# Kernel optimization log

Hardware: AMD Instinct MI355X
Metric: run time of the kernel (lower is better)

The kernel has to match this reference:

```python
import jax, jax.numpy as jnp
import numpy as np

N_NODES = 100000
LN_EPS = 1e-5
NEG_SLOPE = 0.2


def setup_inputs() -> dict:
    key = jax.random.key(0)
    ks = jax.random.split(key, 6)
    N, E, NIN, EDIM, NOUT, H = N_NODES, 1600000, 64, 32, 128, 4
    x = jax.random.normal(ks[0], (N, NIN), dtype=jnp.float32)
    edge_index = jax.random.randint(ks[1], (2, E), 0, N, dtype=jnp.int64)
    edge_attr = jax.random.normal(ks[2], (E, EDIM), dtype=jnp.float32)
    # xavier-uniform linear weights (torch layout: [out, in])
    def xavier(k, fan_out, fan_in):
        lim = float(np.sqrt(6.0 / (fan_in + fan_out)))
        return jax.random.uniform(k, (fan_out, fan_in), jnp.float32, -lim, lim)
    W_msg = xavier(ks[3], NOUT, NIN + EDIM)          # (128, 96)
    W_att = xavier(ks[4], H, 2 * NIN + EDIM)         # (4, 160)
    bias = jnp.zeros((NOUT,), jnp.float32)
    ln_gamma = jnp.ones((NOUT,), jnp.float32)
    ln_beta = jnp.zeros((NOUT,), jnp.float32)
    return {"x": x, "edge_index": edge_index, "edge_attr": edge_attr,
            "W_msg": W_msg, "W_att": W_att, "bias": bias,
            "ln_gamma": ln_gamma, "ln_beta": ln_beta}


def reference(x, edge_index, edge_attr, W_msg, W_att, bias, ln_gamma, ln_beta):
    N = x.shape[0]
    H = W_att.shape[0]
    src, dst = edge_index[0], edge_index[1]
    xs = x[src]                                       # (E, node_in) gather
    xd = x[dst]                                       # (E, node_in) gather
    # message: W_msg @ [h_u ; x_uv]
    msg_in = jnp.concatenate([xs, edge_attr], axis=-1)            # (E, 96)
    msgs = msg_in @ W_msg.T                                        # (E, out_dim)
    msgs = msgs.reshape(-1, H, W_msg.shape[0] // H)                # (E, H, D)
    # attention logits: LeakyReLU(W_att @ [h_u ; h_v ; x_uv])
    att_in = jnp.concatenate([xs, xd, edge_attr], axis=-1)         # (E, 160)
    logits = att_in @ W_att.T                                      # (E, H)
    logits = jax.nn.leaky_relu(logits, NEG_SLOPE)
    # per-destination-node sparse softmax
    seg_max = jax.ops.segment_max(logits, dst, num_segments=N)     # (N, H)
    exp_l = jnp.exp(logits - seg_max[dst])                         # (E, H)
    seg_sum = jax.ops.segment_sum(exp_l, dst, num_segments=N)      # (N, H)
    att = exp_l / (seg_sum[dst] + 1e-9)                            # (E, H)
    # weighted scatter-add aggregation
    weighted = msgs * att[..., None]                               # (E, H, D)
    out = jax.ops.segment_sum(weighted, dst, num_segments=N)       # (N, H, D)
    out = out.reshape(N, -1) + bias                                # concat heads
    # layer norm over feature dim
    mu = out.mean(axis=-1, keepdims=True)
    var = out.var(axis=-1, keepdims=True)
    out = (out - mu) * jax.lax.rsqrt(var + LN_EPS) * ln_gamma + ln_beta
    return out
```

## Files before the change

kernel.cpp:

```cpp
#include <hip/hip_runtime.h>
#include <hip/hip_bf16.h>

typedef __attribute__((ext_vector_type(8))) short short8;
typedef __attribute__((ext_vector_type(4))) float f32x4;

__device__ __forceinline__ unsigned short fbf(float f) {
  union { float f; unsigned u; } v; v.f = f;
  unsigned r = v.u + 0x7fffu + ((v.u >> 16) & 1u);
  return (unsigned short)(r >> 16);
}
__device__ __forceinline__ unsigned pk2(float a, float b) {
  return (unsigned)fbf(a) | ((unsigned)fbf(b) << 16);
}
__device__ __forceinline__ float ubf(unsigned hi) {
  union { unsigned u; float f; } v; v.u = hi << 16; return v.f;
}
__device__ __forceinline__ float dot4(float4 a, float4 b) {
  return fmaf(a.x, b.x, fmaf(a.y, b.y, fmaf(a.z, b.z, a.w * b.w)));
}

__launch_bounds__(256)
__global__ void k_phase1(const float* __restrict__ x, const float* __restrict__ W_att,
                         const int* __restrict__ edst, int E,
                         float4* __restrict__ A_s, float4* __restrict__ A_d,
                         unsigned* __restrict__ xb32, int* __restrict__ deg, int N) {
  __shared__ float4 s_wa[160];
  if (threadIdx.x < 160) s_wa[threadIdx.x] = ((const float4*)W_att)[threadIdx.x];
  for (int i = blockIdx.x * blockDim.x + threadIdx.x; i < E; i += gridDim.x * blockDim.x)
    atomicAdd(&deg[edst[i]], 1);
  __syncthreads();
  for (int v = blockIdx.x * blockDim.x + threadIdx.x; v < N; v += gridDim.x * blockDim.x) {
    const float4* xp = (const float4*)&x[v * 64];
    float4 xq[16];
    #pragma unroll
    for (int k = 0; k < 16; k++) xq[k] = xp[k];
    float as[4] = {}, ad[4] = {};
    #pragma unroll
    for (int h = 0; h < 4; h++) {
      #pragma unroll
      for (int k = 0; k < 16; k++) {
        as[h] += dot4(s_wa[h * 40 + k], xq[k]);
        ad[h] += dot4(s_wa[h * 40 + 16 + k], xq[k]);
      }
    }
    A_s[v] = make_float4(as[0], as[1], as[2], as[3]);
    A_d[v] = make_float4(ad[0], ad[1], ad[2], ad[3]);
    #pragma unroll
    for (int k = 0; k < 16; k++) {
      xb32[v * 32 + 2 * k]     = pk2(xq[k].x, xq[k].y);
      xb32[v * 32 + 2 * k + 1] = pk2(xq[k].z, xq[k].w);
    }
  }
}

__global__ void k_scan1(const int* __restrict__ deg, int N, int* __restrict__ part,
                        int* __restrict__ bsum) {
  __shared__ int tmp[1024];
  int tid = threadIdx.x;
  int i = blockIdx.x * 1024 + tid;
  int dv = (i < N) ? deg[i] : 0;
  int v = (dv + 7) & ~7;
  tmp[tid] = v;
  __syncthreads();
  for (int ofs = 1; ofs < 1024; ofs <<= 1) {
    int t = (tid >= ofs) ? tmp[tid - ofs] : 0;
    __syncthreads();
    tmp[tid] += t;
    __syncthreads();
  }
  if (i < N) part[i] = tmp[tid] - v;
  if (tid == 1023) bsum[blockIdx.x] = tmp[tid];
}

__global__ void k_scan2(int* __restrict__ part, const int* __restrict__ bsum,
                        const int* __restrict__ deg, int N, int* __restrict__ cursor) {
  __shared__ int sbase;
  if (threadIdx.x == 0) {
    int b = 0;
    for (int j = 0; j < (int)blockIdx.x; j++) b += bsum[j];
    sbase = b;
  }
  __syncthreads();
  int i = blockIdx.x * 1024 + threadIdx.x;
  if (i < N) {
    int o = part[i] + sbase;
    part[i] = o;
    cursor[i] = o;
    if (i == N - 1) part[N] = o + ((deg[i] + 7) & ~7);
  }
}

__launch_bounds__(256)
__global__ void k_fill2(const int* __restrict__ esrc, const int* __restrict__ edst, int E,
                        const float* __restrict__ ea, const float4* __restrict__ A_s,
                        const float4* __restrict__ A_d, const float* __restrict__ W_att,
                        int* __restrict__ cursor, int2* __restrict__ csr2,
                        float4* __restrict__ attc) {
  __shared__ float4 s_we[32];
  if (threadIdx.x < 32) {
    int h = threadIdx.x >> 3, k4 = threadIdx.x & 7;
    const float* p = &W_att[h * 160 + 128 + k4 * 4];
    s_we[threadIdx.x] = make_float4(p[0], p[1], p[2], p[3]);
  }
  __syncthreads();
  for (int e = blockIdx.x * blockDim.x + threadIdx.x; e < E; e += gridDim.x * blockDim.x) {
    const int s = esrc[e], d = edst[e];
    const int slot = atomicAdd(&cursor[d], 1);
    const float4* ep = (const float4*)&ea[(unsigned)e * 32u];
    float4 eq[8];
    #pragma unroll
    for (int k = 0; k < 8; k++) eq[k] = ep[k];
    const float4 as4 = A_s[s], ad4 = A_d[d];
    const float base[4] = {as4.x + ad4.x, as4.y + ad4.y, as4.z + ad4.z, as4.w + ad4.w};
    float av[4];
    #pragma unroll
    for (int h = 0; h < 4; h++) {
      float lg = base[h];
      #pragma unroll
      for (int k = 0; k < 8; k++) lg += dot4(s_we[h * 8 + k], eq[k]);
      lg = fmaxf(lg, 0.2f * lg);
      av[h] = __expf(lg);
    }
    attc[slot] = make_float4(av[0], av[1], av[2], av[3]);
    csr2[slot] = make_int2(s, e);
  }
}

__launch_bounds__(256)
__global__ void k_agg2(const unsigned short* __restrict__ xb, const float* __restrict__ ea,
                       const int2* __restrict__ csr2, const float4* __restrict__ attc,
                       const int* __restrict__ offsets,
                       unsigned short* __restrict__ agg, float* __restrict__ denom, int N) {
  __shared__ int2 s_ids[4][32];
  const int lane = threadIdx.x & 63;
  const int wvb = threadIdx.x >> 6;
  const int wv = (blockIdx.x * blockDim.x + threadIdx.x) >> 6;
  const int nw = (gridDim.x * blockDim.x) >> 6;
  const int l32 = lane & 31;
  const bool hi = lane >= 32;

  for (int v0 = wv; v0 < N; v0 += nw) {
    const int vv = __builtin_amdgcn_readfirstlane(v0);
    const int sstart = __builtin_amdgcn_readfirstlane(offsets[vv]);
    const int send = __builtin_amdgcn_readfirstlane(offsets[vv + 1]);
    const int ng = (send - sstart) >> 3;

    float ax0 = 0, ax1 = 0, ax2 = 0, ax3 = 0;
    float ae0 = 0, ae1 = 0, ae2 = 0, ae3 = 0;
    float dn0 = 0, dn1 = 0, dn2 = 0, dn3 = 0;

    if (ng > 0) {
      {
        int2 q_ = csr2[sstart + l32];
        if (lane < 32) s_ids[wvb][l32] = q_;
      }
      for (int g = 0; g < ng; g++) {
        if (g > 0 && (g & 3) == 0) {
          int2 q_ = csr2[sstart + g * 8 + l32];
          if (lane < 32) s_ids[wvb][l32] = q_;
        }
        const int qo = (g & 3) * 8;
        const float4* ap8 = &attc[sstart + g * 8];
        const float4 at0 = ap8[0], at1 = ap8[1], at2 = ap8[2], at3 = ap8[3];
        const float4 at4 = ap8[4], at5 = ap8[5], at6 = ap8[6], at7 = ap8[7];
        const int2 t0 = s_ids[wvb][qo + 0], t1 = s_ids[wvb][qo + 1];
        const int2 t2 = s_ids[wvb][qo + 2], t3 = s_ids[wvb][qo + 3];
        const int2 t4 = s_ids[wvb][qo + 4], t5 = s_ids[wvb][qo + 5];
        const int2 t6 = s_ids[wvb][qo + 6], t7 = s_ids[wvb][qo + 7];
        const unsigned short q0 = xb[(unsigned)(t0.x << 6) + lane];
        const unsigned short q1 = xb[(unsigned)(t1.x << 6) + lane];
        const unsigned short q2 = xb[(unsigned)(t2.x << 6) + lane];
        const unsigned short q3 = xb[(unsigned)(t3.x << 6) + lane];
        const unsigned short q4 = xb[(unsigned)(t4.x << 6) + lane];
        const unsigned short q5 = xb[(unsigned)(t5.x << 6) + lane];
        const unsigned short q6 = xb[(unsigned)(t6.x << 6) + lane];
        const unsigned short q7 = xb[(unsigned)(t7.x << 6) + lane];
        const float e0 = ea[(unsigned)(t0.y << 5) + l32];
        const float e1 = ea[(unsigned)(t1.y << 5) + l32];
        const float e2 = ea[(unsigned)(t2.y << 5) + l32];
        const float e3 = ea[(unsigned)(t3.y << 5) + l32];
        const float e4 = ea[(unsigned)(t4.y << 5) + l32];
        const float e5 = ea[(unsigned)(t5.y << 5) + l32];
        const float e6 = ea[(unsigned)(t6.y << 5) + l32];
        const float e7 = ea[(unsigned)(t7.y << 5) + l32];
        float xf;
#define ACC(AT, Q, EV)                                                      \
        xf = ubf((unsigned)Q);                                              \
        ax0 = fmaf(AT.x, xf, ax0); ax1 = fmaf(AT.y, xf, ax1);               \
        ax2 = fmaf(AT.z, xf, ax2); ax3 = fmaf(AT.w, xf, ax3);               \
        ae0 = fmaf(AT.x, EV, ae0); ae1 = fmaf(AT.y, EV, ae1);               \
        ae2 = fmaf(AT.z, EV, ae2); ae3 = fmaf(AT.w, EV, ae3);               \
        dn0 += AT.x; dn1 += AT.y; dn2 += AT.z; dn3 += AT.w;
        ACC(at0, q0, e0) ACC(at1, q1, e1) ACC(at2, q2, e2) ACC(at3, q3, e3)
        ACC(at4, q4, e4) ACC(at5, q5, e5) ACC(at6, q6, e6) ACC(at7, q7, e7)
#undef ACC
      }
    }

    const unsigned base = (unsigned)v0 * 384u;
    agg[base + lane]        = fbf(ax0);
    agg[base + 96 + lane]   = fbf(ax1);
    agg[base + 192 + lane]  = fbf(ax2);
    agg[base + 288 + lane]  = fbf(ax3);
    const int hA = hi ? 2 : 0;
    agg[base + hA * 96 + 64 + l32]       = fbf(hi ? ae2 : ae0);
    agg[base + (hA + 1) * 96 + 64 + l32] = fbf(hi ? ae3 : ae1);
    if (lane == 0) ((float4*)denom)[v0] = make_float4(dn0, dn1, dn2, dn3);
  }
}

__launch_bounds__(128)
__global__ void k_out(const unsigned short* __restrict__ agg, const float* __restrict__ W_msg,
                      const float* __restrict__ denom, const float* __restrict__ bias,
                      const float* __restrict__ gamma, const float* __restrict__ beta,
                      float* __restrict__ out, int N, int T) {
  __shared__ float s_den[64];
  __shared__ float s_sum[2][16], s_sq[2][16];
  const int f = threadIdx.x;
  const int w = f >> 6;
  const int l = f & 63;
  const int c16 = l & 15;
  const int rg = l >> 4;

  short8 wb[2][2][3];
  float biasv[2][2], gv[2][2], bv[2][2];
  #pragma unroll
  for (int hh = 0; hh < 2; hh++) {
    const int head = 2 * w + hh;
    #pragma unroll
    for (int ct = 0; ct < 2; ct++) {
      const int q = head * 32 + ct * 16 + c16;
      biasv[hh][ct] = bias[q]; gv[hh][ct] = gamma[q]; bv[hh][ct] = beta[q];
      #pragma unroll
      for (int kk = 0; kk < 3; kk++) {
        const float* p = &W_msg[q * 96 + kk * 32 + rg * 8];
        short8 s;
        #pragma unroll
        for (int i = 0; i < 8; i++) s[i] = (short)fbf(p[i]);
        wb[hh][ct][kk] = s;
      }
    }
  }

  for (int t = blockIdx.x; t < T; t += gridDim.x) {
    const int n0 = t * 16;
    if (f < 64) s_den[f] = denom[min(n0 + (f >> 2), N - 1) * 4 + (f & 3)];
    __syncthreads();

    f32x4 c[2][2] = {{{0.f,0.f,0.f,0.f},{0.f,0.f,0.f,0.f}},
                     {{0.f,0.f,0.f,0.f},{0.f,0.f,0.f,0.f}}};
    const int nA = min(n0 + c16, N - 1);
    #pragma unroll
    for (int hh = 0; hh < 2; hh++) {
      const int head = 2 * w + hh;
      #pragma unroll
      for (int kk = 0; kk < 3; kk++) {
        short8 a = *(const short8*)&agg[nA * 384 + head * 96 + kk * 32 + rg * 8];
        c[hh][0] = __builtin_amdgcn_mfma_f32_16x16x32_bf16(a, wb[hh][0][kk], c[hh][0], 0, 0, 0);
        c[hh][1] = __builtin_amdgcn_mfma_f32_16x16x32_bf16(a, wb[hh][1][kk], c[hh][1], 0, 0, 0);
      }
    }

    float val[2][2][4];
    #pragma unroll
    for (int hh = 0; hh < 2; hh++)
      #pragma unroll
      for (int ct = 0; ct < 2; ct++)
        #pragma unroll
        for (int r = 0; r < 4; r++) {
          const float d = s_den[(rg * 4 + r) * 4 + (2 * w + hh)] + 1e-9f;
          val[hh][ct][r] = c[hh][ct][r] / d + biasv[hh][ct];
        }

    float sr[4], qr[4];
    #pragma unroll
    for (int r = 0; r < 4; r++) {
      float s = 0.f, q2 = 0.f;
      #pragma unroll
      for (int hh = 0; hh < 2; hh++)
        #pragma unroll
        for (int ct = 0; ct < 2; ct++) { s += val[hh][ct][r]; q2 = fmaf(val[hh][ct][r], val[hh][ct][r], q2); }
      #pragma unroll
      for (int m = 1; m <= 8; m <<= 1) { s += __shfl_xor(s, m, 64); q2 += __shfl_xor(q2, m, 64); }
      sr[r] = s; qr[r] = q2;
    }
    if (c16 == 0) {
      #pragma unroll
      for (int r = 0; r < 4; r++) { s_sum[w][rg * 4 + r] = sr[r]; s_sq[w][rg * 4 + r] = qr[r]; }
    }
    __syncthreads();

    float mean[4], rstd[4];
    #pragma unroll
    for (int r = 0; r < 4; r++) {
      const int ni = rg * 4 + r;
      mean[r] = (s_sum[0][ni] + s_sum[1][ni]) * (1.f / 128.f);
      const float m2 = (s_sq[0][ni] + s_sq[1][ni]) * (1.f / 128.f);
      rstd[r] = rsqrtf(m2 - mean[r] * mean[r] + 1e-5f);
    }
    #pragma unroll
    for (int hh = 0; hh < 2; hh++)
      #pragma unroll
      for (int ct = 0; ct < 2; ct++)
        #pragma unroll
        for (int r = 0; r < 4; r++) {
          const int n = n0 + rg * 4 + r;
          if (n < N)
            out[n * 128 + (2 * w + hh) * 32 + ct * 16 + c16] =
                (val[hh][ct][r] - mean[r]) * rstd[r] * gv[hh][ct] + bv[hh][ct];
        }
    __syncthreads();
  }
}

extern "C" void kernel_launch(void* const* d_in, const int* in_sizes, int n_in,
                              void* d_out, int out_size, void* d_ws, size_t ws_size,
                              hipStream_t stream) {
  const float* x     = (const float*)d_in[0];
  const int*   ei    = (const int*)d_in[1];
  const float* ea    = (const float*)d_in[2];
  const float* W_msg = (const float*)d_in[3];
  const float* W_att = (const float*)d_in[4];
  const float* bias  = (const float*)d_in[5];
  const float* gamma = (const float*)d_in[6];
  const float* beta  = (const float*)d_in[7];
  float* out = (float*)d_out;

  const int N = in_sizes[0] / 64;
  const int E = in_sizes[1] / 2;
  const int* esrc = ei;
  const int* edst = ei + E;
  const int EP = E + 8 * N + 64;

  char* p = (char*)d_ws;
  int* deg      = (int*)p;            p += (size_t)N * 4;
  int* offsets  = (int*)p;            p += (size_t)(N + 1) * 4;
  int* cursor   = (int*)p;            p += (size_t)N * 4;
  int* bsum     = (int*)p;            p += 2048 * 4;
  int2* csr2    = (int2*)p;           p += (size_t)EP * 8;
  float4* attc  = (float4*)p;         p += (size_t)EP * 16;
  float4* A_s   = (float4*)p;         p += (size_t)N * 16;
  float4* A_d   = (float4*)p;         p += (size_t)N * 16;
  unsigned short* xb = (unsigned short*)p; p += (size_t)N * 64 * 2;
  unsigned short* agg = (unsigned short*)p; p += (size_t)N * 384 * 2;
  float* denom  = (float*)p;

  hipMemsetAsync(deg, 0, (size_t)N * 4, stream);
  hipMemsetAsync(csr2, 0, (size_t)EP * 8, stream);
  hipMemsetAsync(attc, 0, (size_t)EP * 16, stream);
  const int SB = (N + 1023) / 1024;
  const int T = (N + 15) / 16;

  k_phase1<<<2048, 256, 0, stream>>>(x, W_att, edst, E, A_s, A_d, (unsigned*)xb, deg, N);
  k_scan1<<<SB, 1024, 0, stream>>>(deg, N, offsets, bsum);
  k_scan2<<<SB, 1024, 0, stream>>>(offsets, bsum, deg, N, cursor);
  k_fill2<<<2048, 256, 0, stream>>>(esrc, edst, E, ea, A_s, A_d, W_att, cursor, csr2, attc);
  k_agg2<<<2048, 256, 0, stream>>>(xb, ea, csr2, attc, offsets, agg, denom, N);
  k_out<<<T, 128, 0, stream>>>(agg, W_msg, denom, bias, gamma, beta, out, N, T);
}
```

Before: 437.0 us.

## Store attention weights in edge order and pad CSR slots with a sentinel

The fill kernel now writes exp-attention per original edge id (coalesced) instead of scattering into CSR slot order. The aggregation kernel gathers it through the stored edge id. A small pad kernel fills the padding slots with a sentinel edge whose attention is zero, which replaces two large memsets of the CSR and attention buffers. This trades coalesced reads in aggregation for gathered 16-byte reads, while removing scattered writes and memset traffic.

Result: slower. 462.0 us (+5.7%).

```diff
diff --git a/kernel.cpp b/kernel.cpp
--- a/kernel.cpp
+++ b/kernel.cpp
@@ -90,12 +90,24 @@
   }
 }
 
+__global__ void k_pad(const int* __restrict__ offsets, const int* __restrict__ deg,
+                      int2* __restrict__ csr2, float4* __restrict__ att_eo,
+                      int N, int E) {
+  int v = blockIdx.x * blockDim.x + threadIdx.x;
+  if (v == 0) att_eo[E] = make_float4(0.f, 0.f, 0.f, 0.f);
+  if (v < N) {
+    const int o = offsets[v], d = deg[v];
+    const int pe = o + ((d + 7) & ~7);
+    for (int s = o + d; s < pe; s++) csr2[s] = make_int2(0, E);
+  }
+}
+
 __launch_bounds__(256)
-__global__ void k_fill2(const int* __restrict__ esrc, const int* __restrict__ edst, int E,
+__global__ void k_fill3(const int* __restrict__ esrc, const int* __restrict__ edst, int E,
                         const float* __restrict__ ea, const float4* __restrict__ A_s,
                         const float4* __restrict__ A_d, const float* __restrict__ W_att,
                         int* __restrict__ cursor, int2* __restrict__ csr2,
-                        float4* __restrict__ attc) {
+                        float4* __restrict__ att_eo) {
   __shared__ float4 s_we[32];
   if (threadIdx.x < 32) {
     int h = threadIdx.x >> 3, k4 = threadIdx.x & 7;
@@ -121,14 +133,14 @@
       lg = fmaxf(lg, 0.2f * lg);
       av[h] = __expf(lg);
     }
-    attc[slot] = make_float4(av[0], av[1], av[2], av[3]);
+    att_eo[e] = make_float4(av[0], av[1], av[2], av[3]);
     csr2[slot] = make_int2(s, e);
   }
 }
 
 __launch_bounds__(256)
 __global__ void k_agg2(const unsigned short* __restrict__ xb, const float* __restrict__ ea,
-                       const int2* __restrict__ csr2, const float4* __restrict__ attc,
+                       const int2* __restrict__ csr2, const float4* __restrict__ att_eo,
                        const int* __restrict__ offsets,
                        unsigned short* __restrict__ agg, float* __restrict__ denom, int N) {
   __shared__ int2 s_ids[4][32];
@@ -160,13 +172,18 @@
           if (lane < 32) s_ids[wvb][l32] = q_;
         }
         const int qo = (g & 3) * 8;
-        const float4* ap8 = &attc[sstart + g * 8];
-        const float4 at0 = ap8[0], at1 = ap8[1], at2 = ap8[2], at3 = ap8[3];
-        const float4 at4 = ap8[4], at5 = ap8[5], at6 = ap8[6], at7 = ap8[7];
         const int2 t0 = s_ids[wvb][qo + 0], t1 = s_ids[wvb][qo + 1];
         const int2 t2 = s_ids[wvb][qo + 2], t3 = s_ids[wvb][qo + 3];
         const int2 t4 = s_ids[wvb][qo + 4], t5 = s_ids[wvb][qo + 5];
         const int2 t6 = s_ids[wvb][qo + 6], t7 = s_ids[wvb][qo + 7];
+        const float4 at0 = att_eo[(unsigned)t0.y];
+        const float4 at1 = att_eo[(unsigned)t1.y];
+        const float4 at2 = att_eo[(unsigned)t2.y];
+        const float4 at3 = att_eo[(unsigned)t3.y];
+        const float4 at4 = att_eo[(unsigned)t4.y];
+        const float4 at5 = att_eo[(unsigned)t5.y];
+        const float4 at6 = att_eo[(unsigned)t6.y];
+        const float4 at7 = att_eo[(unsigned)t7.y];
         const unsigned short q0 = xb[(unsigned)(t0.x << 6) + lane];
         const unsigned short q1 = xb[(unsigned)(t1.x << 6) + lane];
         const unsigned short q2 = xb[(unsigned)(t2.x << 6) + lane];
@@ -338,7 +355,7 @@
   int* cursor   = (int*)p;            p += (size_t)N * 4;
   int* bsum     = (int*)p;            p += 2048 * 4;
   int2* csr2    = (int2*)p;           p += (size_t)EP * 8;
-  float4* attc  = (float4*)p;         p += (size_t)EP * 16;
+  float4* att_eo = (float4*)p;        p += (size_t)(E + 8) * 16;
   float4* A_s   = (float4*)p;         p += (size_t)N * 16;
   float4* A_d   = (float4*)p;         p += (size_t)N * 16;
   unsigned short* xb = (unsigned short*)p; p += (size_t)N * 64 * 2;
@@ -346,15 +363,14 @@
   float* denom  = (float*)p;
 
   hipMemsetAsync(deg, 0, (size_t)N * 4, stream);
-  hipMemsetAsync(csr2, 0, (size_t)EP * 8, stream);
-  hipMemsetAsync(attc, 0, (size_t)EP * 16, stream);
   const int SB = (N + 1023) / 1024;
   const int T = (N + 15) / 16;
 
   k_phase1<<<2048, 256, 0, stream>>>(x, W_att, edst, E, A_s, A_d, (unsigned*)xb, deg, N);
   k_scan1<<<SB, 1024, 0, stream>>>(deg, N, offsets, bsum);
   k_scan2<<<SB, 1024, 0, stream>>>(offsets, bsum, deg, N, cursor);
-  k_fill2<<<2048, 256, 0, stream>>>(esrc, edst, E, ea, A_s, A_d, W_att, cursor, csr2, attc);
-  k_agg2<<<2048, 256, 0, stream>>>(xb, ea, csr2, attc, offsets, agg, denom, N);
+  k_pad<<<(N + 255) / 256, 256, 0, stream>>>(offsets, deg, csr2, att_eo, N, E);
+  k_fill3<<<2048, 256, 0, stream>>>(esrc, edst, E, ea, A_s, A_d, W_att, cursor, csr2, att_eo);
+  k_agg2<<<2048, 256, 0, stream>>>(xb, ea, csr2, att_eo, offsets, agg, denom, N);
   k_out<<<T, 128, 0, stream>>>(agg, W_msg, denom, bias, gamma, beta, out, N, T);
 }
```

## Pack CSR ids and bf16 attention weights into one int4 record

Applied to the files above, without the earlier changes.

Merges the separate csr2 (src, edge id) and attc (four fp32 attention weights) arrays into a single 16-byte record per slot, storing the weights as packed bf16 pairs. The aggregation kernel now reads these through the shared-memory staging it already used for ids, rather than issuing eight separate float4 loads per group. The two large memsets are dropped; the scan kernel zeroes only the padding slots of each node's segment. This cuts memory traffic and launch count, at the cost of bf16 precision on the attention weights and a serial per-thread padding loop in scan2.

Result: faster. 396.3 us (-9.3%).

```diff
diff --git a/kernel.cpp b/kernel.cpp
--- a/kernel.cpp
+++ b/kernel.cpp
@@ -14,6 +14,12 @@
 }
 __device__ __forceinline__ float ubf(unsigned hi) {
   union { unsigned u; float f; } v; v.u = hi << 16; return v.f;
+}
+__device__ __forceinline__ float ubf_lo(unsigned u) {
+  union { unsigned u; float f; } v; v.u = u << 16; return v.f;
+}
+__device__ __forceinline__ float ubf_hi(unsigned u) {
+  union { unsigned u; float f; } v; v.u = u & 0xffff0000u; return v.f;
 }
 __device__ __forceinline__ float dot4(float4 a, float4 b) {
   return fmaf(a.x, b.x, fmaf(a.y, b.y, fmaf(a.z, b.z, a.w * b.w)));
@@ -73,7 +79,8 @@
 }
 
 __global__ void k_scan2(int* __restrict__ part, const int* __restrict__ bsum,
-                        const int* __restrict__ deg, int N, int* __restrict__ cursor) {
+                        const int* __restrict__ deg, int N, int* __restrict__ cursor,
+                        int4* __restrict__ csrp) {
   __shared__ int sbase;
   if (threadIdx.x == 0) {
     int b = 0;
@@ -83,19 +90,22 @@
   __syncthreads();
   int i = blockIdx.x * 1024 + threadIdx.x;
   if (i < N) {
-    int o = part[i] + sbase;
+    const int o = part[i] + sbase;
     part[i] = o;
     cursor[i] = o;
-    if (i == N - 1) part[N] = o + ((deg[i] + 7) & ~7);
+    const int d = deg[i];
+    const int pe = o + ((d + 7) & ~7);
+    const int4 z = make_int4(0, 0, 0, 0);
+    for (int s = o + d; s < pe; s++) csrp[s] = z;
+    if (i == N - 1) part[N] = pe;
   }
 }
 
 __launch_bounds__(256)
-__global__ void k_fill2(const int* __restrict__ esrc, const int* __restrict__ edst, int E,
+__global__ void k_fillP(const int* __restrict__ esrc, const int* __restrict__ edst, int E,
                         const float* __restrict__ ea, const float4* __restrict__ A_s,
                         const float4* __restrict__ A_d, const float* __restrict__ W_att,
-                        int* __restrict__ cursor, int2* __restrict__ csr2,
-                        float4* __restrict__ attc) {
+                        int* __restrict__ cursor, int4* __restrict__ csrp) {
   __shared__ float4 s_we[32];
   if (threadIdx.x < 32) {
     int h = threadIdx.x >> 3, k4 = threadIdx.x & 7;
@@ -121,17 +131,15 @@
       lg = fmaxf(lg, 0.2f * lg);
       av[h] = __expf(lg);
     }
-    attc[slot] = make_float4(av[0], av[1], av[2], av[3]);
-    csr2[slot] = make_int2(s, e);
+    csrp[slot] = make_int4(s, e, (int)pk2(av[0], av[1]), (int)pk2(av[2], av[3]));
   }
 }
 
 __launch_bounds__(256)
-__global__ void k_agg2(const unsigned short* __restrict__ xb, const float* __restrict__ ea,
-                       const int2* __restrict__ csr2, const float4* __restrict__ attc,
-                       const int* __restrict__ offsets,
+__global__ void k_aggP(const unsigned short* __restrict__ xb, const float* __restrict__ ea,
+                       const int4* __restrict__ csrp, const int* __restrict__ offsets,
                        unsigned short* __restrict__ agg, float* __restrict__ denom, int N) {
-  __shared__ int2 s_ids[4][32];
+  __shared__ int4 s_ids[4][32];
   const int lane = threadIdx.x & 63;
   const int wvb = threadIdx.x >> 6;
   const int wv = (blockIdx.x * blockDim.x + threadIdx.x) >> 6;
@@ -151,22 +159,19 @@
 
     if (ng > 0) {
       {
-        int2 q_ = csr2[sstart + l32];
+        int4 q_ = csrp[sstart + l32];
         if (lane < 32) s_ids[wvb][l32] = q_;
       }
       for (int g = 0; g < ng; g++) {
         if (g > 0 && (g & 3) == 0) {
-          int2 q_ = csr2[sstart + g * 8 + l32];
+          int4 q_ = csrp[sstart + g * 8 + l32];
           if (lane < 32) s_ids[wvb][l32] = q_;
         }
         const int qo = (g & 3) * 8;
-        const float4* ap8 = &attc[sstart + g * 8];
-        const float4 at0 = ap8[0], at1 = ap8[1], at2 = ap8[2], at3 = ap8[3];
-        const float4 at4 = ap8[4], at5 = ap8[5], at6 = ap8[6], at7 = ap8[7];
-        const int2 t0 = s_ids[wvb][qo + 0], t1 = s_ids[wvb][qo + 1];
-        const int2 t2 = s_ids[wvb][qo + 2], t3 = s_ids[wvb][qo + 3];
-        const int2 t4 = s_ids[wvb][qo + 4], t5 = s_ids[wvb][qo + 5];
-        const int2 t6 = s_ids[wvb][qo + 6], t7 = s_ids[wvb][qo + 7];
+        const int4 t0 = s_ids[wvb][qo + 0], t1 = s_ids[wvb][qo + 1];
+        const int4 t2 = s_ids[wvb][qo + 2], t3 = s_ids[wvb][qo + 3];
+        const int4 t4 = s_ids[wvb][qo + 4], t5 = s_ids[wvb][qo + 5];
+        const int4 t6 = s_ids[wvb][qo + 6], t7 = s_ids[wvb][qo + 7];
         const unsigned short q0 = xb[(unsigned)(t0.x << 6) + lane];
         const unsigned short q1 = xb[(unsigned)(t1.x << 6) + lane];
         const unsigned short q2 = xb[(unsigned)(t2.x << 6) + lane];
@@ -183,16 +188,18 @@
         const float e5 = ea[(unsigned)(t5.y << 5) + l32];
         const float e6 = ea[(unsigned)(t6.y << 5) + l32];
         const float e7 = ea[(unsigned)(t7.y << 5) + l32];
-        float xf;
-#define ACC(AT, Q, EV)                                                      \
+        float xf, a0_, a1_, a2_, a3_;
+#define ACC(T, Q, EV)                                                       \
+        a0_ = ubf_lo((unsigned)T.z); a1_ = ubf_hi((unsigned)T.z);           \
+        a2_ = ubf_lo((unsigned)T.w); a3_ = ubf_hi((unsigned)T.w);           \
         xf = ubf((unsigned)Q);                                              \
-        ax0 = fmaf(AT.x, xf, ax0); ax1 = fmaf(AT.y, xf, ax1);               \
-        ax2 = fmaf(AT.z, xf, ax2); ax3 = fmaf(AT.w, xf, ax3);               \
-        ae0 = fmaf(AT.x, EV, ae0); ae1 = fmaf(AT.y, EV, ae1);               \
-        ae2 = fmaf(AT.z, EV, ae2); ae3 = fmaf(AT.w, EV, ae3);               \
-        dn0 += AT.x; dn1 += AT.y; dn2 += AT.z; dn3 += AT.w;
-        ACC(at0, q0, e0) ACC(at1, q1, e1) ACC(at2, q2, e2) ACC(at3, q3, e3)
-        ACC(at4, q4, e4) ACC(at5, q5, e5) ACC(at6, q6, e6) ACC(at7, q7, e7)
+        ax0 = fmaf(a0_, xf, ax0); ax1 = fmaf(a1_, xf, ax1);                 \
+        ax2 = fmaf(a2_, xf, ax2); ax3 = fmaf(a3_, xf, ax3);                 \
+        ae0 = fmaf(a0_, EV, ae0); ae1 = fmaf(a1_, EV, ae1);                 \
+        ae2 = fmaf(a2_, EV, ae2); ae3 = fmaf(a3_, EV, ae3);                 \
+        dn0 += a0_; dn1 += a1_; dn2 += a2_; dn3 += a3_;
+        ACC(t0, q0, e0) ACC(t1, q1, e1) ACC(t2, q2, e2) ACC(t3, q3, e3)
+        ACC(t4, q4, e4) ACC(t5, q5, e5) ACC(t6, q6, e6) ACC(t7, q7, e7)
 #undef ACC
       }
     }
@@ -337,8 +344,7 @@
   int* offsets  = (int*)p;            p += (size_t)(N + 1) * 4;
   int* cursor   = (int*)p;            p += (size_t)N * 4;
   int* bsum     = (int*)p;            p += 2048 * 4;
-  int2* csr2    = (int2*)p;           p += (size_t)EP * 8;
-  float4* attc  = (float4*)p;         p += (size_t)EP * 16;
+  int4* csrp    = (int4*)p;           p += (size_t)EP * 16;
   float4* A_s   = (float4*)p;         p += (size_t)N * 16;
   float4* A_d   = (float4*)p;         p += (size_t)N * 16;
   unsigned short* xb = (unsigned short*)p; p += (size_t)N * 64 * 2;
@@ -346,15 +352,13 @@
   float* denom  = (float*)p;
 
   hipMemsetAsync(deg, 0, (size_t)N * 4, stream);
-  hipMemsetAsync(csr2, 0, (size_t)EP * 8, stream);
-  hipMemsetAsync(attc, 0, (size_t)EP * 16, stream);
   const int SB = (N + 1023) / 1024;
   const int T = (N + 15) / 16;
 
   k_phase1<<<2048, 256, 0, stream>>>(x, W_att, edst, E, A_s, A_d, (unsigned*)xb, deg, N);
   k_scan1<<<SB, 1024, 0, stream>>>(deg, N, offsets, bsum);
-  k_scan2<<<SB, 1024, 0, stream>>>(offsets, bsum, deg, N, cursor);
-  k_fill2<<<2048, 256, 0, stream>>>(esrc, edst, E, ea, A_s, A_d, W_att, cursor, csr2, attc);
-  k_agg2<<<2048, 256, 0, stream>>>(xb, ea, csr2, attc, offsets, agg, denom, N);
+  k_scan2<<<SB, 1024, 0, stream>>>(offsets, bsum, deg, N, cursor, csrp);
+  k_fillP<<<2048, 256, 0, stream>>>(esrc, edst, E, ea, A_s, A_d, W_att, cursor, csrp);
+  k_aggP<<<2048, 256, 0, stream>>>(xb, ea, csrp, offsets, agg, denom, N);
   k_out<<<T, 128, 0, stream>>>(agg, W_msg, denom, bias, gamma, beta, out, N, T);
 }
```
